# Performance work log

Measured on AMD Instinct MI355X. Metric: run time of the kernel, lower is better.

Reference implementation:

```python
import jax, jax.numpy as jnp
import numpy as np
import math

D_MODEL = 512
HEADS = 8
GRID_COUNT = 40000
MAX_LEN = 5000


def _positional_embedding(d_model, max_len=MAX_LEN):
    pe = np.zeros((max_len, d_model), dtype=np.float32)
    position = np.arange(max_len, dtype=np.float32)[:, None]
    div_term = np.exp(np.arange(0, d_model, 2, dtype=np.float32) * -(math.log(10000.0) / d_model))
    pe[:, 0::2] = np.sin(position * div_term)
    pe[:, 1::2] = np.cos(position * div_term)
    return jnp.asarray(pe)  # [max_len, d_model]


def _mha(q, k, v, wq, bq, wk, bk, wv, bv, heads):
    # Faithful to SelfAttention: no 1/sqrt(d_k) scaling in the original.
    B, Sq, D = q.shape
    Sk = k.shape[1]
    dh = D // heads
    Q = (q @ wq.T + bq).reshape(B, Sq, heads, dh)
    K = (k @ wk.T + bk).reshape(B, Sk, heads, dh)
    V = (v @ wv.T + bv).reshape(B, Sk, heads, dh)
    attn = jax.nn.softmax(jnp.einsum('bqhd,bkhd->bhqk', Q, K), axis=-1)
    out = jnp.einsum('bhqk,bkhd->bqhd', attn, V)
    return out.reshape(B, Sq, D)


def setup_inputs() -> dict:
    key = jax.random.key(0)
    ks = jax.random.split(key, 20)
    B, S_CURR, S_HIST, N_MASK = 32, 128, 256, 16
    s = 1.0 / math.sqrt(D_MODEL)

    def lin(k):
        kw, kb = jax.random.split(k)
        w = jax.random.uniform(kw, (D_MODEL, D_MODEL), jnp.float32, -s, s)
        b = jax.random.uniform(kb, (D_MODEL,), jnp.float32, -s, s)
        return w, b

    h_wq, h_bq = lin(ks[0]); h_wk, h_bk = lin(ks[1]); h_wv, h_bv = lin(ks[2])
    c_wq, c_bq = lin(ks[3]); c_wk, c_bk = lin(ks[4]); c_wv, c_bv = lin(ks[5])
    x_wq, x_bq = lin(ks[6]); x_wk, x_bk = lin(ks[7]); x_wv, x_bv = lin(ks[8])
    t2_w, t2_b = lin(ks[9])
    emb = jax.random.normal(ks[10], (GRID_COUNT, D_MODEL), jnp.float32)

    return {
        'hist_traj_grid': jax.random.randint(ks[11], (B, S_HIST), 0, GRID_COUNT),
        'userId': jax.random.randint(ks[12], (B,), 0, 1000),
        'mask_pos': jax.random.randint(ks[13], (B, N_MASK), 0, S_CURR),
        'mask_curr_traj_grid': jax.random.randint(ks[14], (B, S_CURR), 0, GRID_COUNT),
        'aggregator_hist_traj_grid': jax.random.randint(ks[15], (B, S_HIST), 0, GRID_COUNT),
        'emb': emb,
        'h_wq': h_wq, 'h_bq': h_bq, 'h_wk': h_wk, 'h_bk': h_bk, 'h_wv': h_wv, 'h_bv': h_bv,
        'c_wq': c_wq, 'c_bq': c_bq, 'c_wk': c_wk, 'c_bk': c_bk, 'c_wv': c_wv, 'c_bv': c_bv,
        'x_wq': x_wq, 'x_bq': x_bq, 'x_wk': x_wk, 'x_bk': x_bk, 'x_wv': x_wv, 'x_bv': x_bv,
        't2_w': t2_w, 't2_b': t2_b,
    }


def reference(hist_traj_grid, userId, mask_pos, mask_curr_traj_grid, aggregator_hist_traj_grid,
              emb,
              h_wq, h_bq, h_wk, h_bk, h_wv, h_bv,
              c_wq, c_bq, c_wk, c_bk, c_wv, c_bv,
              x_wq, x_bq, x_wk, x_bk, x_wv, x_bv,
              t2_w, t2_b):
    pe = _positional_embedding(D_MODEL)
    hist = emb[aggregator_hist_traj_grid]          # [B, S_hist, D]
    curr = emb[mask_curr_traj_grid]                # [B, S_curr, D]
    hist = hist + pe[None, :hist.shape[1]]
    curr = curr + pe[None, :curr.shape[1]]

    hist = _mha(hist, hist, hist, h_wq, h_bq, h_wk, h_bk, h_wv, h_bv, HEADS)
    curr = _mha(curr, curr, curr, c_wq, c_bq, c_wk, c_bk, c_wv, c_bv, HEADS)
    _cross = _mha(curr, hist, hist, x_wq, x_bq, x_wk, x_bk, x_wv, x_bv, HEADS)
    # NOTE: original overwrites liner_transform output with liner_transform2(tanh(curr)),
    # so cross-attention output and liner_transform do not affect the result.
    hyb = jnp.tanh(curr) @ t2_w.T + t2_b           # [B, S_curr, D]

    # index_select of flattened [B*S, D] at mask_pos + b*S == take_along_axis over seq dim
    gathered = jnp.take_along_axis(hyb, mask_pos[:, :, None], axis=1)  # [B, n_mask, D]
    gathered = gathered.reshape(-1, D_MODEL)

    candidate = emb[2:]                            # [vocab-2, D]
    scores = gathered @ candidate.T                # [B*n_mask, vocab-2]
    return jax.nn.log_softmax(scores, axis=-1)
```

## Files before the change

### kernel.cpp

```cpp
#include <hip/hip_runtime.h>
#include <hip/hip_bf16.h>
#include <math.h>
#include <float.h>

#define B       32
#define S_CURR  128
#define D       512
#define H       8
#define DH      64
#define NM      16
#define NCAND   39998
#define MG      (B * NM)
#define SCLD    40064
#define NT      313

typedef __bf16 bf16x8_t __attribute__((ext_vector_type(8)));
typedef float  f32x4_t  __attribute__((ext_vector_type(4)));

typedef __attribute__((address_space(3))) unsigned int lds_u32_t;
typedef const __attribute__((address_space(1))) unsigned int gbl_u32_t;

__device__ __forceinline__ void async16(const void* g, void* l) {
    __builtin_amdgcn_global_load_lds((gbl_u32_t*)g, (lds_u32_t*)l, 16, 0, 0);
}

__global__ __launch_bounds__(256) void prep_kernel(
    const float* __restrict__ emb,
    const float* __restrict__ wq, const float* __restrict__ wk,
    const float* __restrict__ wv, const float* __restrict__ t2w,
    __bf16* __restrict__ embB, __bf16* __restrict__ wqB, __bf16* __restrict__ wkB,
    __bf16* __restrict__ wvB, __bf16* __restrict__ t2wB,
    const int* __restrict__ curr_idx, __bf16* __restrict__ currB,
    const int* __restrict__ mask_pos, int* __restrict__ qidx)
{
    int bx = blockIdx.x;
    if (bx < 10512) {
        const float* src; __bf16* dst; size_t n, base;
        if (bx < 10000) {
            src = emb + 2 * D; dst = embB; n = (size_t)NCAND * D; base = (size_t)bx * 2048;
        } else {
            int w = (bx - 10000) >> 7;
            base = (size_t)((bx - 10000) & 127) * 2048;
            n = (size_t)D * D;
            src = (w == 0) ? wq : (w == 1) ? wk : (w == 2) ? wv : t2w;
            dst = (w == 0) ? wqB : (w == 1) ? wkB : (w == 2) ? wvB : t2wB;
        }
        size_t i = base + (size_t)threadIdx.x * 8;
        if (i >= n) return;
        float4 a = *(const float4*)(src + i);
        float4 b = *(const float4*)(src + i + 4);
        bf16x8_t v;
        v[0] = (__bf16)a.x; v[1] = (__bf16)a.y; v[2] = (__bf16)a.z; v[3] = (__bf16)a.w;
        v[4] = (__bf16)b.x; v[5] = (__bf16)b.y; v[6] = (__bf16)b.z; v[7] = (__bf16)b.w;
        *(bf16x8_t*)(dst + i) = v;
        return;
    }
    if (bx == 14608) {
        int r = threadIdx.x;
        qidx[r] = (r >> 4) * S_CURR + mask_pos[r];
        r += 256;
        qidx[r] = (r >> 4) * S_CURR + mask_pos[r];
        return;
    }
    int bs = bx - 10512;
    int s = bs & (S_CURR - 1);
    int g = curr_idx[bs];
    const float* e = emb + (size_t)g * D;
    __bf16* o = currB + (size_t)bs * D;
    int d = threadIdx.x * 2;
    float div = expf(-(float)d * (9.210340371976184f / 512.0f));
    float ang = (float)s * div;
    o[d]     = (__bf16)(e[d]     + sinf(ang));
    o[d + 1] = (__bf16)(e[d + 1] + cosf(ang));
}

__global__ __launch_bounds__(256) void gemm_bf(
    const __bf16* __restrict__ A,
    const __bf16* __restrict__ W0, const float* __restrict__ b0, __bf16* __restrict__ C0,
    const __bf16* __restrict__ W1, const float* __restrict__ b1, __bf16* __restrict__ C1,
    const __bf16* __restrict__ W2, const float* __restrict__ b2, __bf16* __restrict__ C2,
    const int* __restrict__ rowidx)
{
    const int z = blockIdx.z;
    if (z == 2 && blockIdx.x >= 4) return;
    const __bf16* W = (z == 0) ? W0 : (z == 1) ? W1 : W2;
    const float* bias = (z == 0) ? b0 : (z == 1) ? b1 : b2;
    __bf16* C = (z == 0) ? C0 : (z == 1) ? C1 : C2;

    __shared__ __bf16 As[128 * 64];
    __shared__ __bf16 Bs[128 * 64];

    const int tid = threadIdx.x, lane = tid & 63, wave = tid >> 6;
    const int wy = wave >> 1, wx = wave & 1;
    const int m0 = blockIdx.x * 128, n0 = blockIdx.y * 128;
    const int lrow = lane >> 3;
    const int lcol = (((lane & 7) ^ lrow) & 7) * 8;

    const __bf16* aptr[4]; const __bf16* bptr[4];
#pragma unroll
    for (int i = 0; i < 4; ++i) {
        int chunk = wave * 4 + i;
        int ar = m0 + chunk * 8 + lrow;
        if (z == 2) ar = rowidx[ar];
        aptr[i] = A + (size_t)ar * 512 + lcol;
        bptr[i] = W + (size_t)(n0 + chunk * 8 + lrow) * 512 + lcol;
    }

    f32x4_t acc[4][4];
#pragma unroll
    for (int i = 0; i < 4; ++i)
#pragma unroll
        for (int j = 0; j < 4; ++j) acc[i][j] = (f32x4_t){0.f, 0.f, 0.f, 0.f};

    const int l7 = lane & 7, quad = lane >> 4, c16 = lane & 15;

    for (int kk = 0; kk < 512; kk += 64) {
#pragma unroll
        for (int i = 0; i < 4; ++i) {
            int chunk = wave * 4 + i;
            async16(aptr[i] + kk, &As[chunk * 512]);
            async16(bptr[i] + kk, &Bs[chunk * 512]);
        }
        __syncthreads();
#pragma unroll
        for (int kb = 0; kb < 2; ++kb) {
            const int goff = (((kb * 4 + quad) ^ l7)) * 8;
            bf16x8_t af[4], bfv[4];
#pragma unroll
            for (int i = 0; i < 4; ++i)
                af[i] = *(const bf16x8_t*)&As[(wy * 64 + i * 16 + c16) * 64 + goff];
#pragma unroll
            for (int j = 0; j < 4; ++j)
                bfv[j] = *(const bf16x8_t*)&Bs[(wx * 64 + j * 16 + c16) * 64 + goff];
#pragma unroll
            for (int i = 0; i < 4; ++i)
#pragma unroll
                for (int j = 0; j < 4; ++j)
                    acc[i][j] = __builtin_amdgcn_mfma_f32_16x16x32_bf16(
                        af[i], bfv[j], acc[i][j], 0, 0, 0);
        }
        __syncthreads();
    }

#pragma unroll
    for (int i = 0; i < 4; ++i)
#pragma unroll
        for (int j = 0; j < 4; ++j) {
            int col = n0 + wx * 64 + j * 16 + c16;
            float bv = bias[col];
#pragma unroll
            for (int rr = 0; rr < 4; ++rr) {
                int row = m0 + wy * 64 + i * 16 + quad * 4 + rr;
                C[(size_t)row * 512 + col] = (__bf16)(acc[i][j][rr] + bv);
            }
        }
}

__global__ __launch_bounds__(256) void gemm_scores(
    const __bf16* __restrict__ A,
    const __bf16* __restrict__ Bm,
    __bf16* __restrict__ scB,
    float* __restrict__ pmax, float* __restrict__ psum)
{
    const int bid = blockIdx.x;
    const int xcd = bid & 7, k = bid >> 3;
    const int nt = xcd * 40 + (k >> 2);
    if (nt >= NT) return;
    const int m0 = (k & 3) * 128, n0 = nt * 128;

    __shared__ __bf16 As[128 * 64];
    __shared__ __bf16 Bs[128 * 64];
    __shared__ float redm[2][128], reds[2][128];

    const int tid = threadIdx.x, lane = tid & 63, wave = tid >> 6;
    const int wy = wave >> 1, wx = wave & 1;
    const int lrow = lane >> 3;
    const int lcol = (((lane & 7) ^ lrow) & 7) * 8;

    const __bf16* aptr[4]; const __bf16* bptr[4];
#pragma unroll
    for (int i = 0; i < 4; ++i) {
        int chunk = wave * 4 + i;
        aptr[i] = A + (size_t)(m0 + chunk * 8 + lrow) * 512 + lcol;
        bptr[i] = Bm + (size_t)(n0 + chunk * 8 + lrow) * 512 + lcol;
    }

    f32x4_t acc[4][4];
#pragma unroll
    for (int i = 0; i < 4; ++i)
#pragma unroll
        for (int j = 0; j < 4; ++j) acc[i][j] = (f32x4_t){0.f, 0.f, 0.f, 0.f};

    const int l7 = lane & 7, quad = lane >> 4, c16 = lane & 15;

    for (int kk = 0; kk < 512; kk += 64) {
#pragma unroll
        for (int i = 0; i < 4; ++i) {
            int chunk = wave * 4 + i;
            async16(aptr[i] + kk, &As[chunk * 512]);
            async16(bptr[i] + kk, &Bs[chunk * 512]);
        }
        __syncthreads();
#pragma unroll
        for (int kb = 0; kb < 2; ++kb) {
            const int goff = (((kb * 4 + quad) ^ l7)) * 8;
            bf16x8_t af[4], bfv[4];
#pragma unroll
            for (int i = 0; i < 4; ++i)
                af[i] = *(const bf16x8_t*)&As[(wy * 64 + i * 16 + c16) * 64 + goff];
#pragma unroll
            for (int j = 0; j < 4; ++j)
                bfv[j] = *(const bf16x8_t*)&Bs[(wx * 64 + j * 16 + c16) * 64 + goff];
#pragma unroll
            for (int i = 0; i < 4; ++i)
#pragma unroll
                for (int j = 0; j < 4; ++j)
                    acc[i][j] = __builtin_amdgcn_mfma_f32_16x16x32_bf16(
                        af[i], bfv[j], acc[i][j], 0, 0, 0);
        }
        __syncthreads();
    }

#pragma unroll
    for (int i = 0; i < 4; ++i) {
#pragma unroll
        for (int rr = 0; rr < 4; ++rr) {
            const int row = wy * 64 + i * 16 + quad * 4 + rr;
            const size_t rowbase = (size_t)(m0 + row) * SCLD;
            float v[4]; float m = -FLT_MAX;
#pragma unroll
            for (int j = 0; j < 4; ++j) {
                int col = n0 + wx * 64 + j * 16 + c16;
                __bf16 xb = (__bf16)acc[i][j][rr];
                if (col < NCAND) {
                    scB[rowbase + col] = xb;
                    float xr = (float)xb;
                    v[j] = xr; m = fmaxf(m, xr);
                } else v[j] = -FLT_MAX;
            }
            float s = 0.f;
#pragma unroll
            for (int j = 0; j < 4; ++j)
                s += (v[j] > -FLT_MAX) ? __expf(v[j] - m) : 0.f;
#pragma unroll
            for (int mk = 1; mk < 16; mk <<= 1) {
                float om = __shfl_xor(m, mk);
                float os = __shfl_xor(s, mk);
                float mm = fmaxf(m, om);
                s = s * __expf(m - mm) + os * __expf(om - mm);
                m = mm;
            }
            if (c16 == 0) { redm[wx][row] = m; reds[wx][row] = s; }
        }
    }
    __syncthreads();
    if (tid < 128) {
        float ma = redm[0][tid], sa = reds[0][tid];
        float mb = redm[1][tid], sb = reds[1][tid];
        float mm = fmaxf(ma, mb);
        float ss = sa * __expf(ma - mm) + sb * __expf(mb - mm);
        pmax[(size_t)nt * MG + m0 + tid] = mm;
        psum[(size_t)nt * MG + m0 + tid] = ss;
    }
}

#define KPAD 72
__global__ __launch_bounds__(256) void attn_kernel(const __bf16* __restrict__ Qg,
                                                   const __bf16* __restrict__ K,
                                                   const __bf16* __restrict__ V,
                                                   __bf16* __restrict__ attnB) {
    const int b = blockIdx.x, h = blockIdx.y, t = threadIdx.x;
    __shared__ __bf16 Ks[128 * KPAD];
    __shared__ __bf16 Vs[128 * KPAD];
    __shared__ float  Qs[16 * 68];
    __shared__ float  P[16 * 130];

    for (int i = t; i < 1024; i += 256) {
        int row = i >> 3, cg = (i & 7) * 8;
        size_t gsrc = ((size_t)(b * S_CURR + row)) * D + h * DH + cg;
        *(bf16x8_t*)&Ks[row * KPAD + cg] = *(const bf16x8_t*)&K[gsrc];
        *(bf16x8_t*)&Vs[row * KPAD + cg] = *(const bf16x8_t*)&V[gsrc];
    }
    if (t < 128) {
        int q = t >> 3, cg = (t & 7) * 8;
        bf16x8_t qv = *(const bf16x8_t*)&Qg[((size_t)(b * NM + q)) * D + h * DH + cg];
#pragma unroll
        for (int u = 0; u < 8; ++u) Qs[q * 68 + cg + u] = (float)qv[u];
    }
    __syncthreads();

    const int q = t >> 4, i = t & 15;
    float sv[8];
    float lmax = -FLT_MAX;
#pragma unroll
    for (int z = 0; z < 8; ++z) {
        int kk = i + z * 16;
        float s = 0.f;
#pragma unroll
        for (int d0 = 0; d0 < DH; d0 += 8) {
            bf16x8_t kv = *(const bf16x8_t*)&Ks[kk * KPAD + d0];
#pragma unroll
            for (int u = 0; u < 8; ++u) s += Qs[q * 68 + d0 + u] * (float)kv[u];
        }
        sv[z] = s; lmax = fmaxf(lmax, s);
    }
#pragma unroll
    for (int mk = 1; mk < 16; mk <<= 1) lmax = fmaxf(lmax, __shfl_xor(lmax, mk));
    float lsum = 0.f;
#pragma unroll
    for (int z = 0; z < 8; ++z) {
        float e = __expf(sv[z] - lmax);
        P[q * 130 + i + z * 16] = e;
        lsum += e;
    }
#pragma unroll
    for (int mk = 1; mk < 16; mk <<= 1) lsum += __shfl_xor(lsum, mk);
    const float inv = 1.0f / lsum;

    const int d = i * 4;
    float a0 = 0.f, a1 = 0.f, a2 = 0.f, a3 = 0.f;
    for (int kk = 0; kk < 128; ++kk) {
        float p = P[q * 130 + kk];
        const __bf16* vr = &Vs[kk * KPAD + d];
        a0 += p * (float)vr[0]; a1 += p * (float)vr[1];
        a2 += p * (float)vr[2]; a3 += p * (float)vr[3];
    }
    __bf16* o = attnB + ((size_t)(b * NM + q)) * D + h * DH + d;
    o[0] = (__bf16)tanhf(a0 * inv); o[1] = (__bf16)tanhf(a1 * inv);
    o[2] = (__bf16)tanhf(a2 * inv); o[3] = (__bf16)tanhf(a3 * inv);
}

__global__ __launch_bounds__(256) void lse_reduce(const float* __restrict__ pmax,
                                                  const float* __restrict__ psum,
                                                  float* __restrict__ lse) {
    int row = blockIdx.x, t = threadIdx.x;
    float m = -FLT_MAX, s = 0.f;
    for (int i = t; i < NT; i += 256) {
        float om = pmax[(size_t)i * MG + row];
        float os = psum[(size_t)i * MG + row];
        float mm = fmaxf(m, om);
        s = s * __expf(m - mm) + os * __expf(om - mm);
        m = mm;
    }
    __shared__ float ms[256], ss[256];
    ms[t] = m; ss[t] = s;
    __syncthreads();
    for (int off = 128; off > 0; off >>= 1) {
        if (t < off) {
            float m1 = ms[t], s1 = ss[t], m2 = ms[t + off], s2 = ss[t + off];
            float mm = fmaxf(m1, m2);
            ms[t] = mm;
            ss[t] = s1 * __expf(m1 - mm) + s2 * __expf(m2 - mm);
        }
        __syncthreads();
    }
    if (t == 0) lse[row] = ms[0] + logf(ss[0]);
}

__global__ __launch_bounds__(256) void final_out(const __bf16* __restrict__ scB,
                                                 const float* __restrict__ lse,
                                                 float* __restrict__ out) {
    int row = blockIdx.y;
    int c0 = (blockIdx.x * 256 + threadIdx.x) * 8;
    if (c0 >= NCAND) return;
    float l = lse[row];
    bf16x8_t v = *(const bf16x8_t*)(scB + (size_t)row * SCLD + c0);
    float* o = out + (size_t)row * NCAND + c0;
    if (c0 + 8 <= NCAND) {
        *(float2*)(o)     = make_float2((float)v[0] - l, (float)v[1] - l);
        *(float2*)(o + 2) = make_float2((float)v[2] - l, (float)v[3] - l);
        *(float2*)(o + 4) = make_float2((float)v[4] - l, (float)v[5] - l);
        *(float2*)(o + 6) = make_float2((float)v[6] - l, (float)v[7] - l);
    } else {
        for (int k2 = 0; k2 < NCAND - c0; ++k2) o[k2] = (float)v[k2] - l;
    }
}

extern "C" void kernel_launch(void* const* d_in, const int* in_sizes, int n_in,
                              void* d_out, int out_size, void* d_ws, size_t ws_size,
                              hipStream_t stream) {
    const int*   mask_pos = (const int*)d_in[2];
    const int*   curr_idx = (const int*)d_in[3];
    const float* emb      = (const float*)d_in[5];
    const float* c_wq = (const float*)d_in[12];
    const float* c_bq = (const float*)d_in[13];
    const float* c_wk = (const float*)d_in[14];
    const float* c_bk = (const float*)d_in[15];
    const float* c_wv = (const float*)d_in[16];
    const float* c_bv = (const float*)d_in[17];
    const float* t2_w = (const float*)d_in[24];
    const float* t2_b = (const float*)d_in[25];
    float* out = (float*)d_out;

    char* w = (char*)d_ws;
    __bf16* embB  = (__bf16*)w;
    __bf16* scB   = (__bf16*)(w + 41025536);
    __bf16* currB = scB;
    __bf16* Kf    = (__bf16*)(w + 41025536 + 4194304);
    __bf16* Vf    = (__bf16*)(w + 41025536 + 8388608);
    __bf16* Qg    = (__bf16*)(w + 41025536 + 12582912);
    __bf16* attnB = (__bf16*)(w + 41025536 + 13107200);
    __bf16* wqB   = (__bf16*)(w + 41025536 + 13631488);
    __bf16* wkB   = (__bf16*)(w + 41025536 + 14155776);
    __bf16* wvB   = (__bf16*)(w + 41025536 + 14680064);
    __bf16* t2wB  = (__bf16*)(w + 41025536 + 15204352);
    int*    qidx  = (int*)   (w + 41025536 + 15728640);
    __bf16* gatheredB = (__bf16*)(w + 82051072);
    float*  pmax  = (float*)(w + 82575360);
    float*  psum  = (float*)(w + 83216384);
    float*  lse   = (float*)(w + 83857408);

    hipLaunchKernelGGL(prep_kernel, dim3(14609), dim3(256), 0, stream,
                       emb, c_wq, c_wk, c_wv, t2_w, embB, wqB, wkB, wvB, t2wB,
                       curr_idx, currB, mask_pos, qidx);
    hipLaunchKernelGGL(gemm_bf, dim3(32, 4, 3), dim3(256), 0, stream,
                       currB, wkB, c_bk, Kf, wvB, c_bv, Vf, wqB, c_bq, Qg, qidx);
    hipLaunchKernelGGL(attn_kernel, dim3(B, H), dim3(256), 0, stream,
                       Qg, Kf, Vf, attnB);
    hipLaunchKernelGGL(gemm_bf, dim3(4, 4, 1), dim3(256), 0, stream,
                       attnB, t2wB, t2_b, gatheredB,
                       t2wB, t2_b, gatheredB, t2wB, t2_b, gatheredB,
                       (const int*)nullptr);
    hipLaunchKernelGGL(gemm_scores, dim3(1280), dim3(256), 0, stream,
                       gatheredB, embB, scB, pmax, psum);
    hipLaunchKernelGGL(lse_reduce, dim3(MG), dim3(256), 0, stream, pmax, psum, lse);
    hipLaunchKernelGGL(final_out, dim3(20, MG), dim3(256), 0, stream, scB, lse, out);
}
```

Measured before the change: 303.2 us.

## Double-buffer LDS tiles in GEMM kernels and vectorize V reads

Both bf16 GEMM kernels now keep two LDS buffers and issue the async global-to-LDS loads for the next K-slice before computing on the current one. Explicit vmcnt/lgkmcnt waits and raw barriers replace __syncthreads so the global loads overlap the MFMA work. This doubles LDS use per block, which may lower occupancy, and relies on hand-counted vmcnt values being correct. Separately, the attention PV loop reads four bf16 V values with one vector load instead of four scalar loads.

```diff
diff --git a/kernel.cpp b/kernel.cpp
--- a/kernel.cpp
+++ b/kernel.cpp
@@ -15,6 +15,7 @@
 #define NT      313
 
 typedef __bf16 bf16x8_t __attribute__((ext_vector_type(8)));
+typedef __bf16 bf16x4_t __attribute__((ext_vector_type(4)));
 typedef float  f32x4_t  __attribute__((ext_vector_type(4)));
 
 typedef __attribute__((address_space(3))) unsigned int lds_u32_t;
@@ -87,8 +88,8 @@
     const float* bias = (z == 0) ? b0 : (z == 1) ? b1 : b2;
     __bf16* C = (z == 0) ? C0 : (z == 1) ? C1 : C2;
 
-    __shared__ __bf16 As[128 * 64];
-    __shared__ __bf16 Bs[128 * 64];
+    __shared__ __bf16 As[2][128 * 64];
+    __shared__ __bf16 Bs[2][128 * 64];
 
     const int tid = threadIdx.x, lane = tid & 63, wave = tid >> 6;
     const int wy = wave >> 1, wx = wave & 1;
@@ -114,24 +115,39 @@
 
     const int l7 = lane & 7, quad = lane >> 4, c16 = lane & 15;
 
-    for (int kk = 0; kk < 512; kk += 64) {
-#pragma unroll
-        for (int i = 0; i < 4; ++i) {
-            int chunk = wave * 4 + i;
-            async16(aptr[i] + kk, &As[chunk * 512]);
-            async16(bptr[i] + kk, &Bs[chunk * 512]);
-        }
-        __syncthreads();
+#pragma unroll
+    for (int i = 0; i < 4; ++i) {
+        int chunk = wave * 4 + i;
+        async16(aptr[i], &As[0][chunk * 512]);
+        async16(bptr[i], &Bs[0][chunk * 512]);
+    }
+
+#pragma unroll
+    for (int t = 0; t < 8; ++t) {
+        const int cur = t & 1;
+        if (t < 7) {
+            const int kk = (t + 1) * 64;
+#pragma unroll
+            for (int i = 0; i < 4; ++i) {
+                int chunk = wave * 4 + i;
+                async16(aptr[i] + kk, &As[cur ^ 1][chunk * 512]);
+                async16(bptr[i] + kk, &Bs[cur ^ 1][chunk * 512]);
+            }
+            asm volatile("s_waitcnt vmcnt(8)" ::: "memory");
+        } else {
+            asm volatile("s_waitcnt vmcnt(0)" ::: "memory");
+        }
+        __builtin_amdgcn_s_barrier();
 #pragma unroll
         for (int kb = 0; kb < 2; ++kb) {
             const int goff = (((kb * 4 + quad) ^ l7)) * 8;
             bf16x8_t af[4], bfv[4];
 #pragma unroll
             for (int i = 0; i < 4; ++i)
-                af[i] = *(const bf16x8_t*)&As[(wy * 64 + i * 16 + c16) * 64 + goff];
+                af[i] = *(const bf16x8_t*)&As[cur][(wy * 64 + i * 16 + c16) * 64 + goff];
 #pragma unroll
             for (int j = 0; j < 4; ++j)
-                bfv[j] = *(const bf16x8_t*)&Bs[(wx * 64 + j * 16 + c16) * 64 + goff];
+                bfv[j] = *(const bf16x8_t*)&Bs[cur][(wx * 64 + j * 16 + c16) * 64 + goff];
 #pragma unroll
             for (int i = 0; i < 4; ++i)
 #pragma unroll
@@ -139,7 +155,8 @@
                     acc[i][j] = __builtin_amdgcn_mfma_f32_16x16x32_bf16(
                         af[i], bfv[j], acc[i][j], 0, 0, 0);
         }
-        __syncthreads();
+        asm volatile("s_waitcnt lgkmcnt(0)" ::: "memory");
+        __builtin_amdgcn_s_barrier();
     }
 
 #pragma unroll
@@ -168,8 +185,8 @@
     if (nt >= NT) return;
     const int m0 = (k & 3) * 128, n0 = nt * 128;
 
-    __shared__ __bf16 As[128 * 64];
-    __shared__ __bf16 Bs[128 * 64];
+    __shared__ __bf16 As[2][128 * 64];
+    __shared__ __bf16 Bs[2][128 * 64];
     __shared__ float redm[2][128], reds[2][128];
 
     const int tid = threadIdx.x, lane = tid & 63, wave = tid >> 6;
@@ -193,24 +210,39 @@
 
     const int l7 = lane & 7, quad = lane >> 4, c16 = lane & 15;
 
-    for (int kk = 0; kk < 512; kk += 64) {
-#pragma unroll
-        for (int i = 0; i < 4; ++i) {
-            int chunk = wave * 4 + i;
-            async16(aptr[i] + kk, &As[chunk * 512]);
-            async16(bptr[i] + kk, &Bs[chunk * 512]);
-        }
-        __syncthreads();
+#pragma unroll
+    for (int i = 0; i < 4; ++i) {
+        int chunk = wave * 4 + i;
+        async16(aptr[i], &As[0][chunk * 512]);
+        async16(bptr[i], &Bs[0][chunk * 512]);
+    }
+
+#pragma unroll
+    for (int t = 0; t < 8; ++t) {
+        const int cur = t & 1;
+        if (t < 7) {
+            const int kk = (t + 1) * 64;
+#pragma unroll
+            for (int i = 0; i < 4; ++i) {
+                int chunk = wave * 4 + i;
+                async16(aptr[i] + kk, &As[cur ^ 1][chunk * 512]);
+                async16(bptr[i] + kk, &Bs[cur ^ 1][chunk * 512]);
+            }
+            asm volatile("s_waitcnt vmcnt(8)" ::: "memory");
+        } else {
+            asm volatile("s_waitcnt vmcnt(0)" ::: "memory");
+        }
+        __builtin_amdgcn_s_barrier();
 #pragma unroll
         for (int kb = 0; kb < 2; ++kb) {
             const int goff = (((kb * 4 + quad) ^ l7)) * 8;
             bf16x8_t af[4], bfv[4];
 #pragma unroll
             for (int i = 0; i < 4; ++i)
-                af[i] = *(const bf16x8_t*)&As[(wy * 64 + i * 16 + c16) * 64 + goff];
+                af[i] = *(const bf16x8_t*)&As[cur][(wy * 64 + i * 16 + c16) * 64 + goff];
 #pragma unroll
             for (int j = 0; j < 4; ++j)
-                bfv[j] = *(const bf16x8_t*)&Bs[(wx * 64 + j * 16 + c16) * 64 + goff];
+                bfv[j] = *(const bf16x8_t*)&Bs[cur][(wx * 64 + j * 16 + c16) * 64 + goff];
 #pragma unroll
             for (int i = 0; i < 4; ++i)
 #pragma unroll
@@ -218,7 +250,8 @@
                     acc[i][j] = __builtin_amdgcn_mfma_f32_16x16x32_bf16(
                         af[i], bfv[j], acc[i][j], 0, 0, 0);
         }
-        __syncthreads();
+        asm volatile("s_waitcnt lgkmcnt(0)" ::: "memory");
+        __builtin_amdgcn_s_barrier();
     }
 
 #pragma unroll
@@ -321,9 +354,9 @@
     float a0 = 0.f, a1 = 0.f, a2 = 0.f, a3 = 0.f;
     for (int kk = 0; kk < 128; ++kk) {
         float p = P[q * 130 + kk];
-        const __bf16* vr = &Vs[kk * KPAD + d];
-        a0 += p * (float)vr[0]; a1 += p * (float)vr[1];
-        a2 += p * (float)vr[2]; a3 += p * (float)vr[3];
+        bf16x4_t vv = *(const bf16x4_t*)&Vs[kk * KPAD + d];
+        a0 += p * (float)vv[0]; a1 += p * (float)vv[1];
+        a2 += p * (float)vv[2]; a3 += p * (float)vv[3];
     }
     __bf16* o = attnB + ((size_t)(b * NM + q)) * D + h * DH + d;
     o[0] = (__bf16)tanhf(a0 * inv); o[1] = (__bf16)tanhf(a1 * inv);
```

Result: no change. 306.1 us (+1.0%).
